# Performance work log

Hardware: AMD Instinct MI355X
Metric: run time of the kernel (lower is better)

The kernel has to match this reference:

```python
import jax, jax.numpy as jnp
import numpy as np

NUM_HEADS = 16
HEAD_DIM = 128
ROT_DIM = 128  # rotary_emb_dim == head_dim
ROPE_BASE = 10000.0


def setup_inputs() -> dict:
    key = jax.random.key(0)
    k1, k2, k3, k4, k5 = jax.random.split(key, 5)
    b, s, d = 2, 2048, 2048
    return {
        "x": jax.random.normal(k1, (b, s, d), jnp.float32),
        "Wqkv_w": jax.random.normal(k2, (3 * d, d), jnp.float32) * (d ** -0.5),
        "Wqkv_b": jax.random.normal(k3, (3 * d,), jnp.float32) * 0.02,
        "wo_w": jax.random.normal(k4, (d, d), jnp.float32) * (d ** -0.5),
        "wo_b": jax.random.normal(k5, (d,), jnp.float32) * 0.02,
    }


def _deinterleave(t):
    # torch.cat([t[..., ::2], t[..., 1::2]], dim=-1)
    return jnp.concatenate([t[..., ::2], t[..., 1::2]], axis=-1)


def _rope(t, cos, sin):
    # non-interleaved (GPT-NeoX style) rotary on first ROT_DIM dims; here ROT_DIM == head_dim
    half = ROT_DIM // 2
    x1, x2 = t[..., :half], t[..., half:ROT_DIM]
    # cos/sin: (s, half) -> broadcast over (b, s, h, half)
    c = cos[None, :, None, :]
    sn = sin[None, :, None, :]
    return jnp.concatenate([x1 * c - x2 * sn, x2 * c + x1 * sn], axis=-1)


def reference(x, Wqkv_w, Wqkv_b, wo_w, wo_b):
    b, s, d = x.shape
    h, hd = NUM_HEADS, HEAD_DIM
    # fused QKV projection, layout '(h three d)' per original rearrange
    qkv = x @ Wqkv_w.T + Wqkv_b                      # (b, s, 3*d)
    qkv = qkv.reshape(b, s, h, 3, hd)
    q = _deinterleave(qkv[:, :, :, 0, :])            # (b, s, h, hd)
    k = _deinterleave(qkv[:, :, :, 1, :])
    v = qkv[:, :, :, 2, :]
    # rotary embedding tables
    inv_freq = 1.0 / (ROPE_BASE ** (jnp.arange(0, ROT_DIM, 2, dtype=jnp.float32) / ROT_DIM))
    freqs = jnp.arange(s, dtype=jnp.float32)[:, None] * inv_freq[None, :]  # (s, half)
    cos, sin = jnp.cos(freqs), jnp.sin(freqs)
    q = _rope(q, cos, sin)
    k = _rope(k, cos, sin)
    # causal self-attention (SelfAttention, softmax_scale = 1/sqrt(hd))
    scale = hd ** -0.5
    scores = jnp.einsum('bshd,bthd->bhst', q, k) * scale  # (b, h, s, s)
    mask = jnp.tril(jnp.ones((s, s), dtype=bool))
    scores = jnp.where(mask[None, None], scores, jnp.finfo(scores.dtype).min)
    probs = jax.nn.softmax(scores, axis=-1)
    ctx = jnp.einsum('bhst,bthd->bshd', probs, v)    # (b, s, h, hd)
    ctx = ctx.reshape(b, s, d)
    return ctx @ wo_w.T + wo_b
```

## Files before the change

kernel.cpp:

```cpp
#include <hip/hip_runtime.h>

#define B_ 2
#define S_ 2048
#define H_ 16
#define HD_ 128
#define QKVROW 6144
#define M_ 4096

typedef float f32x4 __attribute__((ext_vector_type(4)));
typedef __bf16 bf16x8 __attribute__((ext_vector_type(8)));
typedef unsigned short ushortx8 __attribute__((ext_vector_type(8)));

__device__ __forceinline__ float bf2f(unsigned short u) {
  union { unsigned u; float f; } v;
  v.u = ((unsigned)u) << 16;
  return v.f;
}
__device__ __forceinline__ unsigned short f2bf(float f) {
  union { __bf16 b; unsigned short u; } c;
  c.b = (__bf16)f;
  return c.u;
}
__device__ __forceinline__ ushortx8 cvt8(const float* f) {
  const f32x4 lo = *(const f32x4*)f;
  const f32x4 hi = *(const f32x4*)(f + 4);
  ushortx8 o;
#pragma unroll
  for (int t = 0; t < 4; ++t) o[t] = f2bf(lo[t]);
#pragma unroll
  for (int t = 0; t < 4; ++t) o[4 + t] = f2bf(hi[t]);
  return o;
}
__device__ __forceinline__ void async16(const unsigned short* g, unsigned short* l) {
  __builtin_amdgcn_global_load_lds(
      (const __attribute__((address_space(1))) unsigned int*)g,
      (__attribute__((address_space(3))) unsigned int*)l, 16, 0, 0);
}

__global__ __launch_bounds__(256) void gemm1(
    const float* __restrict__ A, const float* __restrict__ Bm,
    const float* __restrict__ bias, unsigned short* __restrict__ C) {
  __shared__ unsigned short As[128 * 64];
  __shared__ unsigned short Bs[128 * 64];
  const int tid = threadIdx.x;
  const int lane = tid & 63, wave = tid >> 6;
  const int l15 = lane & 15, quad = lane >> 4;
  const int m0 = blockIdx.y * 128, n0 = blockIdx.x * 128;
  const int wr = (wave >> 1) * 64, wc = (wave & 1) * 64;

  f32x4 acc[4][4];
#pragma unroll
  for (int r = 0; r < 4; ++r)
#pragma unroll
    for (int c = 0; c < 4; ++c) acc[r][c] = (f32x4){0.f, 0.f, 0.f, 0.f};

  ushortx8 ra[4], rb[4];
#pragma unroll
  for (int p = 0; p < 4; ++p) {
    const int u = p * 256 + tid, row = u >> 3, cu = u & 7;
    ra[p] = cvt8(A + (size_t)(m0 + row) * 2048 + cu * 8);
    rb[p] = cvt8(Bm + (size_t)(n0 + row) * 2048 + cu * 8);
  }

  for (int k0 = 0; k0 < 2048; k0 += 64) {
    __syncthreads();
#pragma unroll
    for (int p = 0; p < 4; ++p) {
      const int u = p * 256 + tid, row = u >> 3, cu = u & 7;
      const int ph = row * 64 + ((cu ^ (row & 7)) << 3);
      *(ushortx8*)&As[ph] = ra[p];
      *(ushortx8*)&Bs[ph] = rb[p];
    }
    __syncthreads();
    if (k0 + 64 < 2048) {
#pragma unroll
      for (int p = 0; p < 4; ++p) {
        const int u = p * 256 + tid, row = u >> 3, cu = u & 7;
        ra[p] = cvt8(A + (size_t)(m0 + row) * 2048 + k0 + 64 + cu * 8);
        rb[p] = cvt8(Bm + (size_t)(n0 + row) * 2048 + k0 + 64 + cu * 8);
      }
    }
#pragma unroll
    for (int s = 0; s < 2; ++s) {
      bf16x8 af[4], bf[4];
#pragma unroll
      for (int r = 0; r < 4; ++r) {
        const int row = wr + r * 16 + l15;
        af[r] = *(const bf16x8*)&As[row * 64 + (((s * 4 + quad) ^ (row & 7)) << 3)];
      }
#pragma unroll
      for (int c = 0; c < 4; ++c) {
        const int row = wc + c * 16 + l15;
        bf[c] = *(const bf16x8*)&Bs[row * 64 + (((s * 4 + quad) ^ (row & 7)) << 3)];
      }
#pragma unroll
      for (int r = 0; r < 4; ++r)
#pragma unroll
        for (int c = 0; c < 4; ++c)
          acc[r][c] = __builtin_amdgcn_mfma_f32_16x16x32_bf16(af[r], bf[c], acc[r][c], 0, 0, 0);
    }
  }

#pragma unroll
  for (int c = 0; c < 4; ++c) {
    const int col = n0 + wc + c * 16 + l15;
    const float bv = bias[col];
#pragma unroll
    for (int r = 0; r < 4; ++r) {
      const int row = m0 + wr + r * 16 + quad * 4;
#pragma unroll
      for (int i = 0; i < 4; ++i)
        C[(size_t)(row + i) * QKVROW + col] = f2bf(acc[r][c][i] + bv);
    }
  }
}

__global__ __launch_bounds__(256) void rope_vt(
    unsigned short* qkv, unsigned short* __restrict__ Vt) {
  __shared__ unsigned short vs[64 * 136];
  const int b = blockIdx.z, h = blockIdx.y, s0 = blockIdx.x * 64;
  const int tid = threadIdx.x;
  const int r = tid >> 2, cpart = (tid & 3) * 32;
  const int s = s0 + r;
  unsigned short* base = qkv + (size_t)(b * S_ + s) * QKVROW + h * 384;
  const int j0 = cpart >> 1;

  ushortx8 ivq[4], ivk[4], ivv[4];
#pragma unroll
  for (int i = 0; i < 4; ++i) {
    ivq[i] = *(const ushortx8*)&base[cpart + i * 8];
    ivk[i] = *(const ushortx8*)&base[128 + cpart + i * 8];
    ivv[i] = *(const ushortx8*)&base[256 + cpart + i * 8];
  }

  float cs[16], sn[16];
#pragma unroll
  for (int t = 0; t < 16; ++t) {
    const float invf = expf(-(float)(j0 + t) * 0.14391156831212787f);
    sincosf((float)s * invf, &sn[t], &cs[t]);
  }

  __syncthreads();

#pragma unroll
  for (int which = 0; which < 2; ++which) {
    const ushortx8* iv = (which == 0) ? ivq : ivk;
    const float scale = (which == 0) ? 0.08838834764831845f : 1.0f;
    ushortx8 o1a, o1b, o2a, o2b;
#pragma unroll
    for (int t = 0; t < 16; ++t) {
      const float x1 = bf2f(iv[(2 * t) >> 3][(2 * t) & 7]);
      const float x2 = bf2f(iv[(2 * t + 1) >> 3][(2 * t + 1) & 7]);
      const unsigned short r1 = f2bf((x1 * cs[t] - x2 * sn[t]) * scale);
      const unsigned short r2 = f2bf((x2 * cs[t] + x1 * sn[t]) * scale);
      if (t < 8) { o1a[t] = r1; o2a[t] = r2; }
      else       { o1b[t - 8] = r1; o2b[t - 8] = r2; }
    }
    unsigned short* out = base + which * 128;
    *(ushortx8*)&out[j0] = o1a;
    *(ushortx8*)&out[j0 + 8] = o1b;
    *(ushortx8*)&out[64 + j0] = o2a;
    *(ushortx8*)&out[64 + j0 + 8] = o2b;
  }

#pragma unroll
  for (int i = 0; i < 4; ++i)
    *(ushortx8*)&vs[r * 136 + cpart + i * 8] = ivv[i];
  __syncthreads();
  const size_t vtb = (size_t)(b * H_ + h) * HD_ * S_ + s0;
#pragma unroll
  for (int it = 0; it < 4; ++it) {
    const int a = tid + it * 256;
    const int d = a >> 3, sc = (a & 7) * 8;
    ushortx8 o;
#pragma unroll
    for (int t = 0; t < 8; ++t) o[t] = vs[(sc + t) * 136 + d];
    *(ushortx8*)&Vt[vtb + (size_t)d * S_ + sc] = o;
  }
}

__global__ __launch_bounds__(512) void attn(
    unsigned short* qkv, const unsigned short* __restrict__ Vt) {
  __shared__ unsigned short Ks[64 * 136];
  __shared__ unsigned short Vs[128 * 72];
  __shared__ unsigned short Ps[8 * 16 * 72];
  const int p = blockIdx.x, bh = blockIdx.y;
  const int b = bh >> 4, h = bh & 15;
  const int tid = threadIdx.x, lane = tid & 63, wave = tid >> 6;
  const int l15 = lane & 15, quad = lane >> 4;

  unsigned short* qh = qkv + (size_t)b * S_ * QKVROW + h * 384;
  const unsigned short* Vb = Vt + (size_t)bh * HD_ * S_;
  unsigned short* Pw = &Ps[wave * 16 * 72];

  ushortx8 rk[2], rv[2];
  auto pref = [&](int j) {
#pragma unroll
    for (int t = 0; t < 2; ++t) {
      const int uk = t * 512 + tid;
      const int krow = uk >> 4, kcu = uk & 15;
      rk[t] = *(const ushortx8*)(qh + (size_t)(j * 64 + krow) * QKVROW + 128 + kcu * 8);
      const int vrow = uk >> 3, vcu = uk & 7;
      rv[t] = *(const ushortx8*)(Vb + (size_t)vrow * S_ + j * 64 + vcu * 8);
    }
  };
  pref(0);

#pragma unroll
  for (int half = 0; half < 2; ++half) {
    const int qt = half ? 15 - p : p;
    const int jN = 2 * qt + 2;

    bf16x8 aq[4];
#pragma unroll
    for (int ks = 0; ks < 4; ++ks)
      aq[ks] = *(const bf16x8*)&qh[(size_t)(qt * 128 + wave * 16 + l15) * QKVROW +
                                   ks * 32 + quad * 8];

    f32x4 o[8];
    float mrow[4], lrow[4];
#pragma unroll
    for (int ct = 0; ct < 8; ++ct) o[ct] = (f32x4){0.f, 0.f, 0.f, 0.f};
#pragma unroll
    for (int i = 0; i < 4; ++i) { mrow[i] = -1e30f; lrow[i] = 0.f; }

    for (int j = 0; j < jN; ++j) {
      __syncthreads();
#pragma unroll
      for (int t = 0; t < 2; ++t) {
        const int uk = t * 512 + tid;
        *(ushortx8*)&Ks[(uk >> 4) * 136 + (uk & 15) * 8] = rk[t];
        *(ushortx8*)&Vs[(uk >> 3) * 72 + (uk & 7) * 8] = rv[t];
      }
      __syncthreads();

      const int jn = (j + 1 < jN) ? j + 1 : (half == 0 ? 0 : -1);
      if (jn >= 0) pref(jn);

      f32x4 sacc[4];
#pragma unroll
      for (int ct = 0; ct < 4; ++ct) sacc[ct] = (f32x4){0.f, 0.f, 0.f, 0.f};
#pragma unroll
      for (int ks = 0; ks < 4; ++ks) {
        bf16x8 bk[4];
#pragma unroll
        for (int ct = 0; ct < 4; ++ct)
          bk[ct] = *(const bf16x8*)&Ks[(ct * 16 + l15) * 136 + ks * 32 + quad * 8];
#pragma unroll
        for (int ct = 0; ct < 4; ++ct)
          sacc[ct] = __builtin_amdgcn_mfma_f32_16x16x32_bf16(aq[ks], bk[ct], sacc[ct], 0, 0, 0);
      }

      if (j >= 2 * qt) {
#pragma unroll
        for (int ct = 0; ct < 4; ++ct)
#pragma unroll
          for (int i = 0; i < 4; ++i) {
            const int grow = qt * 128 + wave * 16 + quad * 4 + i;
            const int gcol = j * 64 + ct * 16 + l15;
            if (gcol > grow) sacc[ct][i] = -1e30f;
          }
      }

#pragma unroll
      for (int i = 0; i < 4; ++i) {
        float m = sacc[0][i];
#pragma unroll
        for (int ct = 1; ct < 4; ++ct) m = fmaxf(m, sacc[ct][i]);
#pragma unroll
        for (int off = 1; off < 16; off <<= 1) m = fmaxf(m, __shfl_xor(m, off));
        const float mn = fmaxf(mrow[i], m);
        const float alpha = __expf(mrow[i] - mn);
        mrow[i] = mn;
        float rsum = 0.f;
#pragma unroll
        for (int ct = 0; ct < 4; ++ct) {
          const float pv = __expf(sacc[ct][i] - mn);
          sacc[ct][i] = pv;
          rsum += pv;
        }
#pragma unroll
        for (int off = 1; off < 16; off <<= 1) rsum += __shfl_xor(rsum, off);
        lrow[i] = lrow[i] * alpha + rsum;
#pragma unroll
        for (int ct = 0; ct < 8; ++ct) o[ct][i] *= alpha;
      }

#pragma unroll
      for (int ct = 0; ct < 4; ++ct)
#pragma unroll
        for (int i = 0; i < 4; ++i)
          Pw[(quad * 4 + i) * 72 + ct * 16 + l15] = f2bf(sacc[ct][i]);

#pragma unroll
      for (int ks = 0; ks < 2; ++ks) {
        const bf16x8 ap = *(const bf16x8*)&Pw[l15 * 72 + ks * 32 + quad * 8];
        bf16x8 bv[8];
#pragma unroll
        for (int ct = 0; ct < 8; ++ct)
          bv[ct] = *(const bf16x8*)&Vs[(ct * 16 + l15) * 72 + ks * 32 + quad * 8];
#pragma unroll
        for (int ct = 0; ct < 8; ++ct)
          o[ct] = __builtin_amdgcn_mfma_f32_16x16x32_bf16(ap, bv[ct], o[ct], 0, 0, 0);
      }
    }

    float inv[4];
#pragma unroll
    for (int i = 0; i < 4; ++i) inv[i] = 1.0f / lrow[i];
#pragma unroll
    for (int ct = 0; ct < 8; ++ct)
#pragma unroll
      for (int i = 0; i < 4; ++i) {
        const int srow = qt * 128 + wave * 16 + quad * 4 + i;
        qh[(size_t)srow * QKVROW + ct * 16 + l15] = f2bf(o[ct][i] * inv[i]);
      }
  }
}

__global__ __launch_bounds__(256) void gemm2(
    const unsigned short* __restrict__ A, const float* __restrict__ Bm,
    const float* __restrict__ bias, float* __restrict__ C) {
  __shared__ unsigned short As[128 * 64];
  __shared__ unsigned short Bs[128 * 64];
  const int tid = threadIdx.x;
  const int lane = tid & 63, wave = tid >> 6;
  const int l15 = lane & 15, quad = lane >> 4;
  const int m0 = blockIdx.y * 128, n0 = blockIdx.x * 128;
  const int wr = (wave >> 1) * 64, wc = (wave & 1) * 64;

  f32x4 acc[4][4];
#pragma unroll
  for (int r = 0; r < 4; ++r)
#pragma unroll
    for (int c = 0; c < 4; ++c) acc[r][c] = (f32x4){0.f, 0.f, 0.f, 0.f};

  ushortx8 rb[4];
#pragma unroll
  for (int p = 0; p < 4; ++p) {
    const int u = p * 256 + tid, row = u >> 3, cu = u & 7;
    rb[p] = cvt8(Bm + (size_t)(n0 + row) * 2048 + cu * 8);
  }

  for (int k0 = 0; k0 < 2048; k0 += 64) {
    const int kh = ((k0 >> 7) * 384) + (k0 & 127);
    __syncthreads();
#pragma unroll
    for (int i = 0; i < 4; ++i) {
      const int c0 = wave * 256 + i * 64;
      const int u = c0 + lane, row = u >> 3, cu = u & 7;
      async16(A + (size_t)(m0 + row) * QKVROW + kh + cu * 8, &As[c0 * 8]);
    }
#pragma unroll
    for (int p = 0; p < 4; ++p) {
      const int u = p * 256 + tid, row = u >> 3, cu = u & 7;
      *(ushortx8*)&Bs[row * 64 + ((cu ^ (row & 7)) << 3)] = rb[p];
    }
    __syncthreads();
    if (k0 + 64 < 2048) {
#pragma unroll
      for (int p = 0; p < 4; ++p) {
        const int u = p * 256 + tid, row = u >> 3, cu = u & 7;
        rb[p] = cvt8(Bm + (size_t)(n0 + row) * 2048 + k0 + 64 + cu * 8);
      }
    }
#pragma unroll
    for (int s = 0; s < 2; ++s) {
      bf16x8 af[4], bf[4];
#pragma unroll
      for (int r = 0; r < 4; ++r)
        af[r] = *(const bf16x8*)&As[(wr + r * 16 + l15) * 64 + (s * 4 + quad) * 8];
#pragma unroll
      for (int c = 0; c < 4; ++c) {
        const int row = wc + c * 16 + l15;
        bf[c] = *(const bf16x8*)&Bs[row * 64 + (((s * 4 + quad) ^ (row & 7)) << 3)];
      }
#pragma unroll
      for (int r = 0; r < 4; ++r)
#pragma unroll
        for (int c = 0; c < 4; ++c)
          acc[r][c] = __builtin_amdgcn_mfma_f32_16x16x32_bf16(af[r], bf[c], acc[r][c], 0, 0, 0);
    }
  }

#pragma unroll
  for (int c = 0; c < 4; ++c) {
    const int col = n0 + wc + c * 16 + l15;
    const float bv = bias[col];
#pragma unroll
    for (int r = 0; r < 4; ++r) {
      const int row = m0 + wr + r * 16 + quad * 4;
#pragma unroll
      for (int i = 0; i < 4; ++i)
        C[(size_t)(row + i) * 2048 + col] = acc[r][c][i] + bv;
    }
  }
}

extern "C" void kernel_launch(void* const* d_in, const int* in_sizes, int n_in,
                              void* d_out, int out_size, void* d_ws, size_t ws_size,
                              hipStream_t stream) {
  const float* x    = (const float*)d_in[0];
  const float* wqkv = (const float*)d_in[1];
  const float* bqkv = (const float*)d_in[2];
  const float* wo   = (const float*)d_in[3];
  const float* bo   = (const float*)d_in[4];
  float* out = (float*)d_out;

  unsigned short* qkv = (unsigned short*)d_ws;
  unsigned short* Vt  = qkv + (size_t)M_ * QKVROW;

  gemm1<<<dim3(QKVROW / 128, M_ / 128), 256, 0, stream>>>(x, wqkv, bqkv, qkv);
  rope_vt<<<dim3(S_ / 64, H_, B_), 256, 0, stream>>>(qkv, Vt);
  attn<<<dim3(8, B_ * H_), 512, 0, stream>>>(qkv, Vt);
  gemm2<<<dim3(2048 / 128, M_ / 128), 256, 0, stream>>>(qkv, wo, bo, out);
}
```

Measured before the change: 488.1 us.

## Pre-convert inputs and weights to bf16 and load GEMM tiles via async LDS

Adds a standalone fp32-to-bf16 conversion kernel that runs over x, Wqkv and Wo into workspace buffers before the GEMMs. Both GEMMs then stream bf16 tiles directly into shared memory with global_load_lds instead of loading fp32, converting in registers and storing to LDS. This cuts repeated fp32 reads and per-tile conversion work, at the cost of extra conversion passes and workspace traffic. The XOR swizzle on the LDS tiles is dropped, so LDS bank conflicts may rise, and register prefetch double-buffering is removed.

```diff
diff --git a/kernel.cpp b/kernel.cpp
--- a/kernel.cpp
+++ b/kernel.cpp
@@ -37,8 +37,18 @@
       (__attribute__((address_space(3))) unsigned int*)l, 16, 0, 0);
 }
 
+__global__ __launch_bounds__(256) void f2bf_arr(
+    const float* __restrict__ src, unsigned short* __restrict__ dst, int n8) {
+  int i = blockIdx.x * 256 + threadIdx.x;
+  const int stride = gridDim.x * 256;
+  for (; i < n8; i += stride) {
+    const ushortx8 o = cvt8(src + (size_t)i * 8);
+    *(ushortx8*)&dst[(size_t)i * 8] = o;
+  }
+}
+
 __global__ __launch_bounds__(256) void gemm1(
-    const float* __restrict__ A, const float* __restrict__ Bm,
+    const unsigned short* __restrict__ A, const unsigned short* __restrict__ Bm,
     const float* __restrict__ bias, unsigned short* __restrict__ C) {
   __shared__ unsigned short As[128 * 64];
   __shared__ unsigned short Bs[128 * 64];
@@ -54,45 +64,27 @@
 #pragma unroll
     for (int c = 0; c < 4; ++c) acc[r][c] = (f32x4){0.f, 0.f, 0.f, 0.f};
 
-  ushortx8 ra[4], rb[4];
-#pragma unroll
-  for (int p = 0; p < 4; ++p) {
-    const int u = p * 256 + tid, row = u >> 3, cu = u & 7;
-    ra[p] = cvt8(A + (size_t)(m0 + row) * 2048 + cu * 8);
-    rb[p] = cvt8(Bm + (size_t)(n0 + row) * 2048 + cu * 8);
-  }
-
   for (int k0 = 0; k0 < 2048; k0 += 64) {
     __syncthreads();
 #pragma unroll
-    for (int p = 0; p < 4; ++p) {
-      const int u = p * 256 + tid, row = u >> 3, cu = u & 7;
-      const int ph = row * 64 + ((cu ^ (row & 7)) << 3);
-      *(ushortx8*)&As[ph] = ra[p];
-      *(ushortx8*)&Bs[ph] = rb[p];
+    for (int i = 0; i < 4; ++i) {
+      const int c0 = wave * 256 + i * 64;
+      const int u = c0 + lane;
+      const int row = u >> 3, cu = u & 7;
+      async16(A + (size_t)(m0 + row) * 2048 + k0 + cu * 8, &As[c0 * 8]);
+      async16(Bm + (size_t)(n0 + row) * 2048 + k0 + cu * 8, &Bs[c0 * 8]);
     }
     __syncthreads();
-    if (k0 + 64 < 2048) {
-#pragma unroll
-      for (int p = 0; p < 4; ++p) {
-        const int u = p * 256 + tid, row = u >> 3, cu = u & 7;
-        ra[p] = cvt8(A + (size_t)(m0 + row) * 2048 + k0 + 64 + cu * 8);
-        rb[p] = cvt8(Bm + (size_t)(n0 + row) * 2048 + k0 + 64 + cu * 8);
-      }
-    }
+
 #pragma unroll
     for (int s = 0; s < 2; ++s) {
       bf16x8 af[4], bf[4];
 #pragma unroll
-      for (int r = 0; r < 4; ++r) {
-        const int row = wr + r * 16 + l15;
-        af[r] = *(const bf16x8*)&As[row * 64 + (((s * 4 + quad) ^ (row & 7)) << 3)];
-      }
-#pragma unroll
-      for (int c = 0; c < 4; ++c) {
-        const int row = wc + c * 16 + l15;
-        bf[c] = *(const bf16x8*)&Bs[row * 64 + (((s * 4 + quad) ^ (row & 7)) << 3)];
-      }
+      for (int r = 0; r < 4; ++r)
+        af[r] = *(const bf16x8*)&As[(wr + r * 16 + l15) * 64 + (s * 4 + quad) * 8];
+#pragma unroll
+      for (int c = 0; c < 4; ++c)
+        bf[c] = *(const bf16x8*)&Bs[(wc + c * 16 + l15) * 64 + (s * 4 + quad) * 8];
 #pragma unroll
       for (int r = 0; r < 4; ++r)
 #pragma unroll
@@ -319,7 +311,7 @@
 }
 
 __global__ __launch_bounds__(256) void gemm2(
-    const unsigned short* __restrict__ A, const float* __restrict__ Bm,
+    const unsigned short* __restrict__ A, const unsigned short* __restrict__ Bm,
     const float* __restrict__ bias, float* __restrict__ C) {
   __shared__ unsigned short As[128 * 64];
   __shared__ unsigned short Bs[128 * 64];
@@ -335,35 +327,19 @@
 #pragma unroll
     for (int c = 0; c < 4; ++c) acc[r][c] = (f32x4){0.f, 0.f, 0.f, 0.f};
 
-  ushortx8 rb[4];
-#pragma unroll
-  for (int p = 0; p < 4; ++p) {
-    const int u = p * 256 + tid, row = u >> 3, cu = u & 7;
-    rb[p] = cvt8(Bm + (size_t)(n0 + row) * 2048 + cu * 8);
-  }
-
   for (int k0 = 0; k0 < 2048; k0 += 64) {
     const int kh = ((k0 >> 7) * 384) + (k0 & 127);
     __syncthreads();
 #pragma unroll
     for (int i = 0; i < 4; ++i) {
       const int c0 = wave * 256 + i * 64;
-      const int u = c0 + lane, row = u >> 3, cu = u & 7;
+      const int u = c0 + lane;
+      const int row = u >> 3, cu = u & 7;
       async16(A + (size_t)(m0 + row) * QKVROW + kh + cu * 8, &As[c0 * 8]);
-    }
-#pragma unroll
-    for (int p = 0; p < 4; ++p) {
-      const int u = p * 256 + tid, row = u >> 3, cu = u & 7;
-      *(ushortx8*)&Bs[row * 64 + ((cu ^ (row & 7)) << 3)] = rb[p];
+      async16(Bm + (size_t)(n0 + row) * 2048 + k0 + cu * 8, &Bs[c0 * 8]);
     }
     __syncthreads();
-    if (k0 + 64 < 2048) {
-#pragma unroll
-      for (int p = 0; p < 4; ++p) {
-        const int u = p * 256 + tid, row = u >> 3, cu = u & 7;
-        rb[p] = cvt8(Bm + (size_t)(n0 + row) * 2048 + k0 + 64 + cu * 8);
-      }
-    }
+
 #pragma unroll
     for (int s = 0; s < 2; ++s) {
       bf16x8 af[4], bf[4];
@@ -371,10 +347,8 @@
       for (int r = 0; r < 4; ++r)
         af[r] = *(const bf16x8*)&As[(wr + r * 16 + l15) * 64 + (s * 4 + quad) * 8];
 #pragma unroll
-      for (int c = 0; c < 4; ++c) {
-        const int row = wc + c * 16 + l15;
-        bf[c] = *(const bf16x8*)&Bs[row * 64 + (((s * 4 + quad) ^ (row & 7)) << 3)];
-      }
+      for (int c = 0; c < 4; ++c)
+        bf[c] = *(const bf16x8*)&Bs[(wc + c * 16 + l15) * 64 + (s * 4 + quad) * 8];
 #pragma unroll
       for (int r = 0; r < 4; ++r)
 #pragma unroll
@@ -409,9 +383,16 @@
 
   unsigned short* qkv = (unsigned short*)d_ws;
   unsigned short* Vt  = qkv + (size_t)M_ * QKVROW;
-
-  gemm1<<<dim3(QKVROW / 128, M_ / 128), 256, 0, stream>>>(x, wqkv, bqkv, qkv);
+  unsigned short* xb  = Vt  + (size_t)B_ * H_ * HD_ * S_;
+  unsigned short* wb  = xb  + (size_t)M_ * 2048;
+  unsigned short* wob = wb  + (size_t)QKVROW * 2048;
+
+  f2bf_arr<<<dim3(2048), 256, 0, stream>>>(x,    xb,  (M_ * 2048) / 8);
+  f2bf_arr<<<dim3(2048), 256, 0, stream>>>(wqkv, wb,  (QKVROW * 2048) / 8);
+  f2bf_arr<<<dim3(1024), 256, 0, stream>>>(wo,   wob, (2048 * 2048) / 8);
+
+  gemm1<<<dim3(QKVROW / 128, M_ / 128), 256, 0, stream>>>(xb, wb, bqkv, qkv);
   rope_vt<<<dim3(S_ / 64, H_, B_), 256, 0, stream>>>(qkv, Vt);
   attn<<<dim3(8, B_ * H_), 512, 0, stream>>>(qkv, Vt);
-  gemm2<<<dim3(2048 / 128, M_ / 128), 256, 0, stream>>>(qkv, wo, bo, out);
-}
+  gemm2<<<dim3(2048 / 128, M_ / 128), 256, 0, stream>>>(qkv, wob, bo, out);
+}
```

New measurement: 447.5 us. 8.3% less time.
